# Performance work log

Measured on AMD Instinct MI355X. Metric: run time of the kernel, lower is better.

## Reference

```python
import jax, jax.numpy as jnp
import numpy as np
from jax import lax

# Module constants (from init_kwargs)
B, C = 2, 64            # batch, in_channel
H, W, D = 64, 64, 64    # size
GROUPS = 2


def setup_inputs() -> dict:
    key = jax.random.key(0)
    ks = jax.random.split(key, 4)
    x = jax.random.normal(ks[0], (B, H * W * D, C), dtype=jnp.float32)
    # TransverseConv: Conv3d(2, W*2, (H,3,3), pad (0,1,1)) -> weight (O,I,kD,kH,kW)
    w_t = jax.random.normal(ks[1], (W * GROUPS, GROUPS, H, 3, 3), dtype=jnp.float32) * 0.02
    b_t = jnp.zeros((W * GROUPS,), jnp.float32)
    # CoronalConv: Conv3d(2, W*2, (3,3,D), pad (1,1,0))
    w_c = jax.random.normal(ks[2], (W * GROUPS, GROUPS, 3, 3, D), dtype=jnp.float32) * 0.02
    b_c = jnp.zeros((W * GROUPS,), jnp.float32)
    # map: Conv3d(2C, C, 1) stored as dense (C, 2C)
    w_map = jax.random.normal(ks[3], (C, 2 * C), dtype=jnp.float32) * 0.02
    b_map = jnp.zeros((C,), jnp.float32)
    return {"x": x, "w_t": w_t, "b_t": b_t, "w_c": w_c, "b_c": b_c,
            "w_map": w_map, "b_map": b_map}


def _forward(x, w_t, b_t, w_c, b_c, w_map, b_map):
    Bx, N, Cx = x.shape
    xg = x.transpose(0, 2, 1).reshape(Bx, Cx, H, W, D)   # (B,C,H,W,D)
    shortcut = xg
    xr = xg.reshape(Bx * Cx // GROUPS, GROUPS, H, W, D)
    dn = ('NCDHW', 'OIDHW', 'NCDHW')
    # Transverse: kernel spans full H -> output (B*C/2, 2W, 1, W, D)
    tans = lax.conv_general_dilated(xr, w_t, (1, 1, 1), [(0, 0), (1, 1), (1, 1)],
                                    dimension_numbers=dn)
    tans = tans + b_t[None, :, None, None, None]
    tans = tans.reshape(Bx, Cx, W, W, D)                 # (B,C,W,W,D)
    # Coronal: kernel spans full D -> output (B*C/2, 2W, H, W, 1)
    cor = lax.conv_general_dilated(xr, w_c, (1, 1, 1), [(1, 1), (1, 1), (0, 0)],
                                   dimension_numbers=dn)
    cor = cor + b_c[None, :, None, None, None]
    cor = cor.reshape(Bx, Cx, W, H, W)                   # (B,C,W,H,W)
    t1 = tans.transpose(0, 1, 3, 2, 4)                   # (B,C,W,W,D)
    c1 = cor.transpose(0, 1, 4, 3, 2)                    # (B,C,W,H,W)
    f = jnp.matmul(c1, t1).transpose(0, 1, 3, 2, 4)      # (B,C,H,W,D)
    attn = jnp.matmul(cor, tans).transpose(0, 1, 3, 2, 4)  # (B,C,H,W,D)
    cat = jnp.concatenate([shortcut * f, attn], axis=1)  # (B,2C,H,W,D)
    mapped = jnp.einsum('bkhwd,ck->bchwd', cat, w_map) + b_map[None, :, None, None, None]
    out = jax.nn.gelu(mapped, approximate=False)         # torch nn.GELU = exact erf
    return out.reshape(Bx, Cx, -1).transpose(0, 2, 1)    # (B,N,C)


def reference(x, w_t, b_t, w_c, b_c, w_map, b_map):
    return _forward(x, w_t, b_t, w_c, b_c, w_map, b_map)
```

## Files before the change

### kernel.cpp

```cpp
#include <hip/hip_runtime.h>
#include <hip/hip_bf16.h>
#include <math.h>

#define HWD 262144

typedef __attribute__((ext_vector_type(8))) short bf16x8;
typedef __attribute__((ext_vector_type(16))) float f32x16;

__device__ inline unsigned short bfu(float f) {
    __hip_bfloat16 h = __float2bfloat16(f);
    return *reinterpret_cast<unsigned short*>(&h);
}

__global__ void k_prep(const float* __restrict__ w_t, const float* __restrict__ w_c,
                       const float* __restrict__ w_map,
                       __hip_bfloat16* __restrict__ A_t, __hip_bfloat16* __restrict__ A_c,
                       __hip_bfloat16* __restrict__ Wb) {
    int i = blockIdx.x * 256 + threadIdx.x;
    if (i < 147456) {
        int kk = i & 15, oc = (i >> 4) & 127, ks = i >> 11;
        int z4 = ks & 3, kq = ks >> 2;
        int g = kq / 9, tap = kq - 9 * g;
        int z = z4 * 16 + kk;
        A_t[i] = __float2bfloat16(w_t[((oc * 2 + g) * 64 + z) * 9 + tap]);
        A_c[i] = __float2bfloat16(w_c[((oc * 2 + g) * 9 + tap) * 64 + z]);
    }
    if (i < 8192) {
        Wb[i] = __float2bfloat16(w_map[i]);
    }
}

__device__ inline void pack_row_bf16(__hip_bfloat16* dst, const float* src) {
    unsigned short u[16];
#pragma unroll
    for (int j = 0; j < 16; ++j) u[j] = bfu(src[j]);
    uint4* q = reinterpret_cast<uint4*>(dst);
    q[0] = *reinterpret_cast<const uint4*>(&u[0]);
    q[1] = *reinterpret_cast<const uint4*>(&u[8]);
}

__global__ void k_trans_c(const float* __restrict__ x, __hip_bfloat16* __restrict__ Xc) {
    __shared__ unsigned short tile[256][68];
    int b = blockIdx.y;
    long n0 = (long)blockIdx.x * 256;
    int t = threadIdx.x;
    const float4* xp4 = (const float4*)(x + ((long)b * HWD + n0) * 64);
#pragma unroll
    for (int i = 0; i < 16; ++i) {
        int f4i = i * 256 + t;
        float4 v = xp4[f4i];
        int nl = f4i >> 4, c4 = (f4i & 15) * 4;
        ushort4 u;
        u.x = bfu(v.x); u.y = bfu(v.y); u.z = bfu(v.z); u.w = bfu(v.w);
        *(ushort4*)&tile[nl][c4] = u;
    }
    __syncthreads();
    int c = t >> 2, hwl = t & 3;
    int hw0 = blockIdx.x * 4;
    __hip_bfloat16* dst0 = Xc + (long)(b * 64 + c) * HWD + (long)(hw0 + hwl) * 16;
#pragma unroll
    for (int z4 = 0; z4 < 4; ++z4) {
        unsigned short u[16];
#pragma unroll
        for (int j = 0; j < 16; ++j) u[j] = tile[hwl * 64 + z4 * 16 + j][c];
        __hip_bfloat16* dst = dst0 + z4 * 65536;
        *(uint4*)dst = *(const uint4*)&u[0];
        *(uint4*)(dst + 8) = *(const uint4*)&u[8];
    }
}

__global__ void k_trans_t(const float* __restrict__ x, __hip_bfloat16* __restrict__ Xt) {
    __shared__ unsigned short tile[256][68];
    int b = blockIdx.y;
    int wd0 = blockIdx.x * 4;
    int t = threadIdx.x;
    const float* xb = x + (long)b * HWD * 64 + (long)wd0 * 64;
#pragma unroll
    for (int i = 0; i < 16; ++i) {
        int idx = i * 256 + t;
        int h = idx >> 6, f = idx & 63;
        float4 v = *(const float4*)(xb + (long)h * 262144 + f * 4);
        int wdl = f >> 4, c4 = (f & 15) * 4;
        ushort4 u;
        u.x = bfu(v.x); u.y = bfu(v.y); u.z = bfu(v.z); u.w = bfu(v.w);
        *(ushort4*)&tile[wdl * 64 + h][c4] = u;
    }
    __syncthreads();
    int c = t >> 2, wdl = t & 3;
    __hip_bfloat16* dst0 = Xt + (long)(b * 64 + c) * HWD + (long)(wd0 + wdl) * 16;
#pragma unroll
    for (int z4 = 0; z4 < 4; ++z4) {
        unsigned short u[16];
#pragma unroll
        for (int j = 0; j < 16; ++j) u[j] = tile[wdl * 64 + z4 * 16 + j][c];
        __hip_bfloat16* dst = dst0 + z4 * 65536;
        *(uint4*)dst = *(const uint4*)&u[0];
        *(uint4*)(dst + 8) = *(const uint4*)&u[8];
    }
}

struct Frag { uint4 a0[4], a1[4], b0[4], b1[4]; };

__global__ __launch_bounds__(256, 2) void k_conv_mfma(
        const __hip_bfloat16* __restrict__ X, const __hip_bfloat16* __restrict__ Aglob,
        const float* __restrict__ bias, float* __restrict__ Out) {
    int L = blockIdx.x;
    int grp = (L & 7) * 8 + ((L >> 3) >> 5);
    int pt = (L >> 3) & 31;
    int b = grp >> 5, ch = grp & 31;
    int p0 = pt * 2;
    const short* Xg = (const short*)(X + ((long)(b * 64 + 2 * ch)) * HWD);
    const short* Ag = (const short*)Aglob;
    int t = threadIdx.x;
    int lane = t & 63, wv = t >> 6;
    int O0 = (wv >> 1) * 64;
    int N0 = (wv & 1) * 64;
    int lrow = lane & 31, lq = lane >> 5;
    int pr = N0 >> 6;

    f32x16 acc00 = {0}, acc01 = {0}, acc10 = {0}, acc11 = {0};

    const short* Ap = Ag + (O0 + lrow) * 16 + lq * 8;
    const short* XgL = Xg + lrow * 16 + lq * 8;
    const uint4 zero4 = {0u, 0u, 0u, 0u};

    auto loadKq = [&](int kq, Frag& f) {
        int g = (kq >= 9) ? 1 : 0;
        int tap = kq - 9 * g;
        int r = tap / 3, s = tap - 3 * r;
        int pp = p0 + pr + r - 1;
        bool pok = (unsigned)pp < 64u;
        bool q0ok = pok && ((s > 0) || (lrow != 0));
        bool q1ok = pok && ((s < 2) || (lrow != 31));
        const short* px = XgL + ((long)g * HWD + pp * 1024 + (s - 1) * 16);
#pragma unroll
        for (int z4 = 0; z4 < 4; ++z4) {
            int ks = kq * 4 + z4;
            f.b0[z4] = q0ok ? *(const uint4*)(px + z4 * 65536) : zero4;
            f.b1[z4] = q1ok ? *(const uint4*)(px + z4 * 65536 + 512) : zero4;
            f.a0[z4] = *(const uint4*)(Ap + ks * 2048);
            f.a1[z4] = *(const uint4*)(Ap + ks * 2048 + 512);
        }
    };
    auto mfmaKq = [&](Frag& f) {
#pragma unroll
        for (int z4 = 0; z4 < 4; ++z4) {
            bf16x8 a0 = *(bf16x8*)&f.a0[z4];
            bf16x8 a1 = *(bf16x8*)&f.a1[z4];
            bf16x8 b0 = *(bf16x8*)&f.b0[z4];
            bf16x8 b1 = *(bf16x8*)&f.b1[z4];
            acc00 = __builtin_amdgcn_mfma_f32_32x32x16_bf16(a0, b0, acc00, 0, 0, 0);
            acc01 = __builtin_amdgcn_mfma_f32_32x32x16_bf16(a0, b1, acc01, 0, 0, 0);
            acc10 = __builtin_amdgcn_mfma_f32_32x32x16_bf16(a1, b0, acc10, 0, 0, 0);
            acc11 = __builtin_amdgcn_mfma_f32_32x32x16_bf16(a1, b1, acc11, 0, 0, 0);
        }
    };

    Frag fA, fB;
    loadKq(0, fA);
#pragma unroll
    for (int k2 = 0; k2 < 9; ++k2) {
        loadKq(2 * k2 + 1, fB);
        mfmaKq(fA);
        if (2 * k2 + 2 < 18) loadKq(2 * k2 + 2, fA);
        mfmaKq(fB);
    }

    long base0 = ((long)(b * 64 + 2 * ch)) * HWD + (long)p0 * 64;
    int n0l = N0 + lrow, n1l = N0 + 32 + lrow;
    long noff0 = (long)(n0l >> 6) * 64 + (n0l & 63);
    long noff1 = (long)(n1l >> 6) * 64 + (n1l & 63);
#pragma unroll
    for (int reg = 0; reg < 16; ++reg) {
        int row = (reg & 3) + 8 * (reg >> 2) + 4 * lq;
        int oc0 = O0 + row, oc1 = O0 + 32 + row;
        long cb0 = base0 + (long)(oc0 >> 6) * HWD + (long)(oc0 & 63) * 4096;
        long cb1 = base0 + (long)(oc1 >> 6) * HWD + (long)(oc1 & 63) * 4096;
        float bs0 = bias[oc0], bs1 = bias[oc1];
        Out[cb0 + noff0] = acc00[reg] + bs0;
        Out[cb0 + noff1] = acc01[reg] + bs0;
        Out[cb1 + noff0] = acc10[reg] + bs1;
        Out[cb1 + noff1] = acc11[reg] + bs1;
    }
}

__global__ __launch_bounds__(128) void k_attn(const float* __restrict__ Cc,
        const float* __restrict__ T, __hip_bfloat16* __restrict__ At) {
    __shared__ float As[64][65];
    __shared__ float Bs[64][64];
    int bc = blockIdx.x >> 6, w2 = blockIdx.x & 63;
    const float4* Ap4 = (const float4*)(Cc + ((long)bc * 64 + w2) * 4096);
    const float4* Bp4 = (const float4*)(T + ((long)bc * 64 + w2) * 4096);
    int t = threadIdx.x;
#pragma unroll
    for (int i = 0; i < 8; ++i) {
        int f = i * 128 + t;
        int r = f >> 4, q4 = (f & 15) * 4;
        float4 v = Ap4[f];
        As[r][q4 + 0] = v.x; As[r][q4 + 1] = v.y; As[r][q4 + 2] = v.z; As[r][q4 + 3] = v.w;
        float4 w = Bp4[f];
        *(float4*)&Bs[r][q4] = w;
    }
    __syncthreads();
    int h2 = t >> 2, dg = (t & 3) * 16;
    f32x16 acc0 = {0}, acc1 = {0};
    for (int k = 0; k < 64; ++k) {
        float a0 = As[h2][k];
        float a1 = As[h2 + 32][k];
        const float* br = &Bs[k][dg];
#pragma unroll
        for (int i = 0; i < 16; ++i) {
            acc0[i] = fmaf(a0, br[i], acc0[i]);
            acc1[i] = fmaf(a1, br[i], acc1[i]);
        }
    }
    float tmp[16];
    __hip_bfloat16* Ab = At + (long)bc * HWD + (long)h2 * 4096 + w2 * 64 + dg;
#pragma unroll
    for (int i = 0; i < 16; ++i) tmp[i] = acc0[i];
    pack_row_bf16(Ab, tmp);
#pragma unroll
    for (int i = 0; i < 16; ++i) tmp[i] = acc1[i];
    pack_row_bf16(Ab + 32L * 4096, tmp);
}

__global__ __launch_bounds__(512, 4) void k_f(const float* __restrict__ Cc,
        const float* __restrict__ T, __hip_bfloat16* __restrict__ F) {
    __shared__ float As[16][64][8];
    __shared__ float Bs[16][8][68];
    int L = blockIdx.x;
    int xcd = L & 7, j = L >> 3;
    int bc = xcd * 16 + (j >> 3), wt = j & 7;
    const float* Ab = Cc + (long)bc * HWD + wt * 8;
    const float* Bb = T + (long)bc * HWD + wt * 8 * 64;
    int t = threadIdx.x;
    int w = t & 7, h = t >> 3;
    f32x16 acc0 = {0}, acc1 = {0}, acc2 = {0}, acc3 = {0};

    for (int w2c = 0; w2c < 4; ++w2c) {
        __syncthreads();
#pragma unroll
        for (int i = 0; i < 4; ++i) {
            int f = i * 512 + t;
            int half = f & 1, hh = (f >> 1) & 63, kk = f >> 7;
            float4 v = *(const float4*)(Ab + (long)(w2c * 16 + kk) * 4096 + hh * 64 + half * 4);
            *(float4*)&As[kk][hh][half * 4] = v;
        }
#pragma unroll
        for (int i = 0; i < 4; ++i) {
            int f = i * 512 + t;
            int d4 = f & 15, ww = (f >> 4) & 7, kk = f >> 7;
            float4 v = *(const float4*)(Bb + (long)(w2c * 16 + kk) * 4096 + ww * 64 + d4 * 4);
            *(float4*)&Bs[kk][ww][d4 * 4] = v;
        }
        __syncthreads();
        for (int kk = 0; kk < 16; ++kk) {
            float a = As[kk][h][w];
            const float* br = &Bs[kk][w][0];
#pragma unroll
            for (int i = 0; i < 16; ++i) {
                acc0[i] = fmaf(a, br[i], acc0[i]);
                acc1[i] = fmaf(a, br[16 + i], acc1[i]);
                acc2[i] = fmaf(a, br[32 + i], acc2[i]);
                acc3[i] = fmaf(a, br[48 + i], acc3[i]);
            }
        }
    }
    __hip_bfloat16* Fp = F + (long)bc * HWD + (long)h * 4096 + (wt * 8 + w) * 64;
    float tmp[16];
#pragma unroll
    for (int i = 0; i < 16; ++i) tmp[i] = acc0[i];
    pack_row_bf16(Fp, tmp);
#pragma unroll
    for (int i = 0; i < 16; ++i) tmp[i] = acc1[i];
    pack_row_bf16(Fp + 16, tmp);
#pragma unroll
    for (int i = 0; i < 16; ++i) tmp[i] = acc2[i];
    pack_row_bf16(Fp + 32, tmp);
#pragma unroll
    for (int i = 0; i < 16; ++i) tmp[i] = acc3[i];
    pack_row_bf16(Fp + 48, tmp);
}

__global__ __launch_bounds__(256, 4) void k_map(const float* __restrict__ x,
        const __hip_bfloat16* __restrict__ F, const __hip_bfloat16* __restrict__ At,
        const __hip_bfloat16* __restrict__ Wb, const float* __restrict__ b_map,
        float* __restrict__ out) {
    __shared__ float xs[16][257];
    __shared__ __hip_bfloat16 fa[16][264];
    __shared__ short Pl[256][24];
    __shared__ short Wt[64][136];

    int t = threadIdx.x;
    long n0 = (long)blockIdx.x * 256;
    int b = (int)(n0 >> 18);
    long nn0 = n0 & (HWD - 1);
    const float* xblk = x + n0 * 64;
    const __hip_bfloat16* Fb = F + (long)b * 64 * HWD + nn0;
    const __hip_bfloat16* Ab = At + (long)b * 64 * HWD + nn0;

#pragma unroll
    for (int i = 0; i < 4; ++i) {
        int e = i * 256 + t;
        int c = e >> 4, kk = (e & 15) * 8;
        *(uint4*)&Wt[c][kk] = *(const uint4*)((const short*)Wb + c * 128 + kk);
    }

    int lane = t & 63, wv = t >> 6;
    int lrow = lane & 31, lhalf = lane >> 5;
    f32x16 acc00 = {0}, acc01 = {0}, acc10 = {0}, acc11 = {0};

    for (int kc = 0; kc < 8; ++kc) {
        __syncthreads();
        if (kc < 4) {
#pragma unroll
            for (int i2 = 0; i2 < 4; ++i2) {
                int f = i2 * 256 + t;
                int nr = f >> 2, j4 = (f & 3) * 4;
                float4 v = *(const float4*)(xblk + nr * 64 + kc * 16 + j4);
                xs[j4 + 0][nr] = v.x;
                xs[j4 + 1][nr] = v.y;
                xs[j4 + 2][nr] = v.z;
                xs[j4 + 3][nr] = v.w;
            }
#pragma unroll
            for (int it = 0; it < 2; ++it) {
                int idx = it * 256 + t;
                int row = idx >> 5, seg = idx & 31;
                *(uint4*)&fa[row][seg * 8] =
                    *(const uint4*)(Fb + (long)(kc * 16 + row) * HWD + seg * 8);
            }
        } else {
#pragma unroll
            for (int it = 0; it < 2; ++it) {
                int idx = it * 256 + t;
                int row = idx >> 5, seg = idx & 31;
                *(uint4*)&fa[row][seg * 8] =
                    *(const uint4*)(Ab + (long)((kc - 4) * 16 + row) * HWD + seg * 8);
            }
        }
        __syncthreads();
        unsigned short pv[16];
        if (kc < 4) {
#pragma unroll
            for (int k2 = 0; k2 < 16; ++k2) {
                float p = xs[k2][t] * __bfloat162float(fa[k2][t]);
                pv[k2] = bfu(p);
            }
        } else {
#pragma unroll
            for (int k2 = 0; k2 < 16; ++k2)
                pv[k2] = *reinterpret_cast<const unsigned short*>(&fa[k2][t]);
        }
        *(uint4*)&Pl[t][0] = *(uint4*)&pv[0];
        *(uint4*)&Pl[t][8] = *(uint4*)&pv[8];
        __syncthreads();
        bf16x8 a0 = *(const bf16x8*)&Pl[wv * 64 + lrow][lhalf * 8];
        bf16x8 a1 = *(const bf16x8*)&Pl[wv * 64 + 32 + lrow][lhalf * 8];
        bf16x8 b0 = *(const bf16x8*)&Wt[lrow][kc * 16 + lhalf * 8];
        bf16x8 b1 = *(const bf16x8*)&Wt[32 + lrow][kc * 16 + lhalf * 8];
        acc00 = __builtin_amdgcn_mfma_f32_32x32x16_bf16(a0, b0, acc00, 0, 0, 0);
        acc01 = __builtin_amdgcn_mfma_f32_32x32x16_bf16(a0, b1, acc01, 0, 0, 0);
        acc10 = __builtin_amdgcn_mfma_f32_32x32x16_bf16(a1, b0, acc10, 0, 0, 0);
        acc11 = __builtin_amdgcn_mfma_f32_32x32x16_bf16(a1, b1, acc11, 0, 0, 0);
    }

    float bs0 = b_map[lrow];
    float bs1 = b_map[32 + lrow];
    const float inv_sqrt2 = 0.70710678118654752440f;
    float* ob = out + (n0 + wv * 64) * 64;
#pragma unroll
    for (int reg = 0; reg < 16; ++reg) {
        int nrow = (reg & 3) + 8 * (reg >> 2) + 4 * lhalf;
        float v00 = acc00[reg] + bs0;
        float v01 = acc01[reg] + bs1;
        float v10 = acc10[reg] + bs0;
        float v11 = acc11[reg] + bs1;
        v00 = 0.5f * v00 * (1.f + erff(v00 * inv_sqrt2));
        v01 = 0.5f * v01 * (1.f + erff(v01 * inv_sqrt2));
        v10 = 0.5f * v10 * (1.f + erff(v10 * inv_sqrt2));
        v11 = 0.5f * v11 * (1.f + erff(v11 * inv_sqrt2));
        ob[(long)nrow * 64 + lrow] = v00;
        ob[(long)nrow * 64 + 32 + lrow] = v01;
        ob[(long)(32 + nrow) * 64 + lrow] = v10;
        ob[(long)(32 + nrow) * 64 + 32 + lrow] = v11;
    }
}

extern "C" void kernel_launch(void* const* d_in, const int* in_sizes, int n_in,
                              void* d_out, int out_size, void* d_ws, size_t ws_size,
                              hipStream_t stream) {
    const float* x     = (const float*)d_in[0];
    const float* w_t   = (const float*)d_in[1];
    const float* b_t   = (const float*)d_in[2];
    const float* w_c   = (const float*)d_in[3];
    const float* b_c   = (const float*)d_in[4];
    const float* w_map = (const float*)d_in[5];
    const float* b_map = (const float*)d_in[6];
    float* out = (float*)d_out;
    float* ws = (float*)d_ws;

    __hip_bfloat16* Xc = (__hip_bfloat16*)ws;
    __hip_bfloat16* Xt = (__hip_bfloat16*)(ws + 16777216L);
    float* T = ws + 33554432L;
    float* Cc = out;
    __hip_bfloat16* A_t = (__hip_bfloat16*)(ws + 67108864L);
    __hip_bfloat16* A_c = (__hip_bfloat16*)(ws + 67182592L);
    __hip_bfloat16* Wb = (__hip_bfloat16*)(ws + 67256320L);
    __hip_bfloat16* At_bf = Xc;
    __hip_bfloat16* F_bf = Xt;

    hipLaunchKernelGGL(k_prep, dim3(576), dim3(256), 0, stream, w_t, w_c, w_map, A_t, A_c, Wb);
    hipLaunchKernelGGL(k_trans_c, dim3(1024, 2), dim3(256), 0, stream, x, Xc);
    hipLaunchKernelGGL(k_trans_t, dim3(1024, 2), dim3(256), 0, stream, x, Xt);
    hipLaunchKernelGGL(k_conv_mfma, dim3(2048), dim3(256), 0, stream, Xt, A_t, b_t, T);
    hipLaunchKernelGGL(k_conv_mfma, dim3(2048), dim3(256), 0, stream, Xc, A_c, b_c, Cc);
    hipLaunchKernelGGL(k_attn, dim3(8192), dim3(128), 0, stream, Cc, T, At_bf);
    hipLaunchKernelGGL(k_f, dim3(1024), dim3(512), 0, stream, Cc, T, F_bf);
    hipLaunchKernelGGL(k_map, dim3(2048), dim3(256), 0, stream, x, F_bf, At_bf, Wb, b_map, out);
}
```

Baseline: 802.1 us.

## Stage conv input tiles in double-buffered LDS and enlarge per-block spatial tile

The conv MFMA kernel now cooperatively loads the shifted input (B operand) tile into double-buffered shared memory once per tap and reads it from LDS for all waves. Each block covers four output rows instead of two, and each wave computes a 64x128 output tile with eight accumulators. This halves the grid and lets a block reuse weight fragments across more columns. In return it adds a __syncthreads per tap and LDS traffic, raises register pressure, and removes the previous register-level prefetch of the A fragments.

```diff
diff --git a/kernel.cpp b/kernel.cpp
--- a/kernel.cpp
+++ b/kernel.cpp
@@ -99,88 +99,104 @@
     }
 }
 
-struct Frag { uint4 a0[4], a1[4], b0[4], b1[4]; };
-
 __global__ __launch_bounds__(256, 2) void k_conv_mfma(
         const __hip_bfloat16* __restrict__ X, const __hip_bfloat16* __restrict__ Aglob,
         const float* __restrict__ bias, float* __restrict__ Out) {
     int L = blockIdx.x;
-    int grp = (L & 7) * 8 + ((L >> 3) >> 5);
-    int pt = (L >> 3) & 31;
+    int grp = (L & 7) * 8 + ((L >> 3) >> 4);
+    int pt = (L >> 3) & 15;
     int b = grp >> 5, ch = grp & 31;
-    int p0 = pt * 2;
+    int p0 = pt * 4;
     const short* Xg = (const short*)(X + ((long)(b * 64 + 2 * ch)) * HWD);
     const short* Ag = (const short*)Aglob;
     int t = threadIdx.x;
     int lane = t & 63, wv = t >> 6;
     int O0 = (wv >> 1) * 64;
-    int N0 = (wv & 1) * 64;
+    int N0 = (wv & 1) * 128;
     int lrow = lane & 31, lq = lane >> 5;
-    int pr = N0 >> 6;
-
-    f32x16 acc00 = {0}, acc01 = {0}, acc10 = {0}, acc11 = {0};
-
-    const short* Ap = Ag + (O0 + lrow) * 16 + lq * 8;
-    const short* XgL = Xg + lrow * 16 + lq * 8;
+
+    __shared__ __align__(16) short Bsm[2][4][2][2048];
+
+    f32x16 acc[2][4];
+#pragma unroll
+    for (int m = 0; m < 2; ++m)
+#pragma unroll
+        for (int j = 0; j < 4; ++j) acc[m][j] = (f32x16){0};
+
+    int srow0 = t >> 1, srow1 = 128 + (t >> 1), shalf = t & 1;
     const uint4 zero4 = {0u, 0u, 0u, 0u};
-
-    auto loadKq = [&](int kq, Frag& f) {
+    uint4 ld[8];
+
+    auto stage_load = [&](int kq) {
         int g = (kq >= 9) ? 1 : 0;
         int tap = kq - 9 * g;
         int r = tap / 3, s = tap - 3 * r;
-        int pp = p0 + pr + r - 1;
-        bool pok = (unsigned)pp < 64u;
-        bool q0ok = pok && ((s > 0) || (lrow != 0));
-        bool q1ok = pok && ((s < 2) || (lrow != 31));
-        const short* px = XgL + ((long)g * HWD + pp * 1024 + (s - 1) * 16);
+        int pr0 = srow0 >> 6, q0 = srow0 & 63;
+        int pr1 = srow1 >> 6, q1 = srow1 & 63;
+        int pp0 = p0 + pr0 + r - 1, qq0 = q0 + s - 1;
+        int pp1 = p0 + pr1 + r - 1, qq1 = q1 + s - 1;
+        bool ok0 = ((unsigned)pp0 < 64u) && ((unsigned)qq0 < 64u);
+        bool ok1 = ((unsigned)pp1 < 64u) && ((unsigned)qq1 < 64u);
+        const short* px0 = Xg + (long)g * HWD + (pp0 * 64 + qq0) * 16 + shalf * 8;
+        const short* px1 = Xg + (long)g * HWD + (pp1 * 64 + qq1) * 16 + shalf * 8;
+#pragma unroll
+        for (int z4 = 0; z4 < 4; ++z4) {
+            ld[2 * z4 + 0] = ok0 ? *(const uint4*)(px0 + z4 * 65536) : zero4;
+            ld[2 * z4 + 1] = ok1 ? *(const uint4*)(px1 + z4 * 65536) : zero4;
+        }
+    };
+    auto stage_write = [&](int buf) {
+#pragma unroll
+        for (int z4 = 0; z4 < 4; ++z4) {
+            *(uint4*)&Bsm[buf][z4][shalf][srow0 * 8] = ld[2 * z4 + 0];
+            *(uint4*)&Bsm[buf][z4][shalf][srow1 * 8] = ld[2 * z4 + 1];
+        }
+    };
+
+    stage_load(0);
+    stage_write(0);
+    __syncthreads();
+
+    int buf = 0;
+    for (int kq = 0; kq < 18; ++kq) {
+        if (kq < 17) stage_load(kq + 1);
 #pragma unroll
         for (int z4 = 0; z4 < 4; ++z4) {
             int ks = kq * 4 + z4;
-            f.b0[z4] = q0ok ? *(const uint4*)(px + z4 * 65536) : zero4;
-            f.b1[z4] = q1ok ? *(const uint4*)(px + z4 * 65536 + 512) : zero4;
-            f.a0[z4] = *(const uint4*)(Ap + ks * 2048);
-            f.a1[z4] = *(const uint4*)(Ap + ks * 2048 + 512);
-        }
-    };
-    auto mfmaKq = [&](Frag& f) {
-#pragma unroll
-        for (int z4 = 0; z4 < 4; ++z4) {
-            bf16x8 a0 = *(bf16x8*)&f.a0[z4];
-            bf16x8 a1 = *(bf16x8*)&f.a1[z4];
-            bf16x8 b0 = *(bf16x8*)&f.b0[z4];
-            bf16x8 b1 = *(bf16x8*)&f.b1[z4];
-            acc00 = __builtin_amdgcn_mfma_f32_32x32x16_bf16(a0, b0, acc00, 0, 0, 0);
-            acc01 = __builtin_amdgcn_mfma_f32_32x32x16_bf16(a0, b1, acc01, 0, 0, 0);
-            acc10 = __builtin_amdgcn_mfma_f32_32x32x16_bf16(a1, b0, acc10, 0, 0, 0);
-            acc11 = __builtin_amdgcn_mfma_f32_32x32x16_bf16(a1, b1, acc11, 0, 0, 0);
-        }
-    };
-
-    Frag fA, fB;
-    loadKq(0, fA);
-#pragma unroll
-    for (int k2 = 0; k2 < 9; ++k2) {
-        loadKq(2 * k2 + 1, fB);
-        mfmaKq(fA);
-        if (2 * k2 + 2 < 18) loadKq(2 * k2 + 2, fA);
-        mfmaKq(fB);
+            const short* Apk = Ag + ks * 2048 + (O0 + lrow) * 16 + lq * 8;
+            uint4 a0u = *(const uint4*)(Apk);
+            uint4 a1u = *(const uint4*)(Apk + 512);
+            bf16x8 a0 = *(bf16x8*)&a0u;
+            bf16x8 a1 = *(bf16x8*)&a1u;
+#pragma unroll
+            for (int j = 0; j < 4; ++j) {
+                bf16x8 bj = *(const bf16x8*)&Bsm[buf][z4][lq][(N0 + 32 * j + lrow) * 8];
+                acc[0][j] = __builtin_amdgcn_mfma_f32_32x32x16_bf16(a0, bj, acc[0][j], 0, 0, 0);
+                acc[1][j] = __builtin_amdgcn_mfma_f32_32x32x16_bf16(a1, bj, acc[1][j], 0, 0, 0);
+            }
+        }
+        if (kq < 17) {
+            stage_write(buf ^ 1);
+            __syncthreads();
+            buf ^= 1;
+        }
     }
 
     long base0 = ((long)(b * 64 + 2 * ch)) * HWD + (long)p0 * 64;
-    int n0l = N0 + lrow, n1l = N0 + 32 + lrow;
-    long noff0 = (long)(n0l >> 6) * 64 + (n0l & 63);
-    long noff1 = (long)(n1l >> 6) * 64 + (n1l & 63);
 #pragma unroll
     for (int reg = 0; reg < 16; ++reg) {
         int row = (reg & 3) + 8 * (reg >> 2) + 4 * lq;
-        int oc0 = O0 + row, oc1 = O0 + 32 + row;
-        long cb0 = base0 + (long)(oc0 >> 6) * HWD + (long)(oc0 & 63) * 4096;
-        long cb1 = base0 + (long)(oc1 >> 6) * HWD + (long)(oc1 & 63) * 4096;
-        float bs0 = bias[oc0], bs1 = bias[oc1];
-        Out[cb0 + noff0] = acc00[reg] + bs0;
-        Out[cb0 + noff1] = acc01[reg] + bs0;
-        Out[cb1 + noff0] = acc10[reg] + bs1;
-        Out[cb1 + noff1] = acc11[reg] + bs1;
+#pragma unroll
+        for (int m = 0; m < 2; ++m) {
+            int oc = O0 + 32 * m + row;
+            long cb = base0 + (long)(oc >> 6) * HWD + (long)(oc & 63) * 4096;
+            float bs = bias[oc];
+#pragma unroll
+            for (int j = 0; j < 4; ++j) {
+                int nn = N0 + 32 * j + lrow;
+                Out[cb + nn] = acc[m][j][reg] + bs;
+            }
+        }
     }
 }
 
@@ -413,8 +429,8 @@
     hipLaunchKernelGGL(k_prep, dim3(576), dim3(256), 0, stream, w_t, w_c, w_map, A_t, A_c, Wb);
     hipLaunchKernelGGL(k_trans_c, dim3(1024, 2), dim3(256), 0, stream, x, Xc);
     hipLaunchKernelGGL(k_trans_t, dim3(1024, 2), dim3(256), 0, stream, x, Xt);
-    hipLaunchKernelGGL(k_conv_mfma, dim3(2048), dim3(256), 0, stream, Xt, A_t, b_t, T);
-    hipLaunchKernelGGL(k_conv_mfma, dim3(2048), dim3(256), 0, stream, Xc, A_c, b_c, Cc);
+    hipLaunchKernelGGL(k_conv_mfma, dim3(1024), dim3(256), 0, stream, Xt, A_t, b_t, T);
+    hipLaunchKernelGGL(k_conv_mfma, dim3(1024), dim3(256), 0, stream, Xc, A_c, b_c, Cc);
     hipLaunchKernelGGL(k_attn, dim3(8192), dim3(128), 0, stream, Cc, T, At_bf);
     hipLaunchKernelGGL(k_f, dim3(1024), dim3(512), 0, stream, Cc, T, F_bf);
     hipLaunchKernelGGL(k_map, dim3(2048), dim3(256), 0, stream, x, F_bf, At_bf, Wb, b_map, out);
```

After: 1.028 ms. 1.28x slower.

## Stage conv input tiles through double-buffered LDS instead of per-wave global loads

Applied to the files above, without the earlier changes.

The conv MFMA kernel now loads each tap's X tile cooperatively into a double-buffered shared-memory array once per block and reads B fragments from LDS. Before, each wave fetched its own fragments from global memory, and waves sharing the same columns loaded them redundantly. The register-prefetched fragment pipeline for A is removed, A is now loaded directly each step, and launch bounds go from 2 to 3 blocks per SM. The cost is a __syncthreads per K step and exposed A-load latency.

```diff
diff --git a/kernel.cpp b/kernel.cpp
--- a/kernel.cpp
+++ b/kernel.cpp
@@ -99,9 +99,7 @@
     }
 }
 
-struct Frag { uint4 a0[4], a1[4], b0[4], b1[4]; };
-
-__global__ __launch_bounds__(256, 2) void k_conv_mfma(
+__global__ __launch_bounds__(256, 3) void k_conv_mfma(
         const __hip_bfloat16* __restrict__ X, const __hip_bfloat16* __restrict__ Aglob,
         const float* __restrict__ bias, float* __restrict__ Out) {
     int L = blockIdx.x;
@@ -116,54 +114,62 @@
     int O0 = (wv >> 1) * 64;
     int N0 = (wv & 1) * 64;
     int lrow = lane & 31, lq = lane >> 5;
-    int pr = N0 >> 6;
+
+    __shared__ __align__(16) short Bsm[2][4][2][1024];
 
     f32x16 acc00 = {0}, acc01 = {0}, acc10 = {0}, acc11 = {0};
 
-    const short* Ap = Ag + (O0 + lrow) * 16 + lq * 8;
-    const short* XgL = Xg + lrow * 16 + lq * 8;
+    int srow = t >> 1, shalf = t & 1;
+    int spr = srow >> 6, sq = srow & 63;
     const uint4 zero4 = {0u, 0u, 0u, 0u};
-
-    auto loadKq = [&](int kq, Frag& f) {
+    uint4 ld0, ld1, ld2, ld3;
+
+    auto stage_load = [&](int kq) {
         int g = (kq >= 9) ? 1 : 0;
         int tap = kq - 9 * g;
         int r = tap / 3, s = tap - 3 * r;
-        int pp = p0 + pr + r - 1;
-        bool pok = (unsigned)pp < 64u;
-        bool q0ok = pok && ((s > 0) || (lrow != 0));
-        bool q1ok = pok && ((s < 2) || (lrow != 31));
-        const short* px = XgL + ((long)g * HWD + pp * 1024 + (s - 1) * 16);
+        int pp = p0 + spr + r - 1, qq = sq + s - 1;
+        bool ok = ((unsigned)pp < 64u) && ((unsigned)qq < 64u);
+        const short* px = Xg + (long)g * HWD + (pp * 64 + qq) * 16 + shalf * 8;
+        ld0 = ok ? *(const uint4*)(px)           : zero4;
+        ld1 = ok ? *(const uint4*)(px + 65536)   : zero4;
+        ld2 = ok ? *(const uint4*)(px + 131072)  : zero4;
+        ld3 = ok ? *(const uint4*)(px + 196608)  : zero4;
+    };
+    auto stage_write = [&](int buf) {
+        *(uint4*)&Bsm[buf][0][shalf][srow * 8] = ld0;
+        *(uint4*)&Bsm[buf][1][shalf][srow * 8] = ld1;
+        *(uint4*)&Bsm[buf][2][shalf][srow * 8] = ld2;
+        *(uint4*)&Bsm[buf][3][shalf][srow * 8] = ld3;
+    };
+
+    stage_load(0);
+    stage_write(0);
+    __syncthreads();
+
+    int buf = 0;
+    for (int kq = 0; kq < 18; ++kq) {
+        if (kq < 17) stage_load(kq + 1);
 #pragma unroll
         for (int z4 = 0; z4 < 4; ++z4) {
             int ks = kq * 4 + z4;
-            f.b0[z4] = q0ok ? *(const uint4*)(px + z4 * 65536) : zero4;
-            f.b1[z4] = q1ok ? *(const uint4*)(px + z4 * 65536 + 512) : zero4;
-            f.a0[z4] = *(const uint4*)(Ap + ks * 2048);
-            f.a1[z4] = *(const uint4*)(Ap + ks * 2048 + 512);
-        }
-    };
-    auto mfmaKq = [&](Frag& f) {
-#pragma unroll
-        for (int z4 = 0; z4 < 4; ++z4) {
-            bf16x8 a0 = *(bf16x8*)&f.a0[z4];
-            bf16x8 a1 = *(bf16x8*)&f.a1[z4];
-            bf16x8 b0 = *(bf16x8*)&f.b0[z4];
-            bf16x8 b1 = *(bf16x8*)&f.b1[z4];
+            const short* Apk = Ag + ks * 2048 + (O0 + lrow) * 16 + lq * 8;
+            uint4 a0u = *(const uint4*)(Apk);
+            uint4 a1u = *(const uint4*)(Apk + 512);
+            bf16x8 a0 = *(bf16x8*)&a0u;
+            bf16x8 a1 = *(bf16x8*)&a1u;
+            bf16x8 b0 = *(const bf16x8*)&Bsm[buf][z4][lq][(N0 + lrow) * 8];
+            bf16x8 b1 = *(const bf16x8*)&Bsm[buf][z4][lq][(N0 + 32 + lrow) * 8];
             acc00 = __builtin_amdgcn_mfma_f32_32x32x16_bf16(a0, b0, acc00, 0, 0, 0);
             acc01 = __builtin_amdgcn_mfma_f32_32x32x16_bf16(a0, b1, acc01, 0, 0, 0);
             acc10 = __builtin_amdgcn_mfma_f32_32x32x16_bf16(a1, b0, acc10, 0, 0, 0);
             acc11 = __builtin_amdgcn_mfma_f32_32x32x16_bf16(a1, b1, acc11, 0, 0, 0);
         }
-    };
-
-    Frag fA, fB;
-    loadKq(0, fA);
-#pragma unroll
-    for (int k2 = 0; k2 < 9; ++k2) {
-        loadKq(2 * k2 + 1, fB);
-        mfmaKq(fA);
-        if (2 * k2 + 2 < 18) loadKq(2 * k2 + 2, fA);
-        mfmaKq(fB);
+        if (kq < 17) {
+            stage_write(buf ^ 1);
+            __syncthreads();
+            buf ^= 1;
+        }
     }
 
     long base0 = ((long)(b * 64 + 2 * ch)) * HWD + (long)p0 * 64;
```

Measured after the change: 780.9 us. -2.6%, faster.
